# Optimization experiments

Measured on AMD Instinct MI355X. Metric: run time of the kernel, lower is better.

## Reference

```python
import jax, jax.numpy as jnp
import numpy as np

N = 8192       # num_nodes
E = 262144     # num_edges (avg degree 32)
D_IN = 256
D_H = 256
D_OUT = 256
BN_EPS = 1e-5


def _linear_params(key, din, dout):
    # torch nn.Linear default init: U(-1/sqrt(din), 1/sqrt(din))
    s = 1.0 / np.sqrt(din)
    kw, kb = jax.random.split(key)
    W = jax.random.uniform(kw, (dout, din), jnp.float32, -s, s)
    b = jax.random.uniform(kb, (dout,), jnp.float32, -s, s)
    return W, b


def setup_inputs() -> dict:
    key = jax.random.key(0)
    ks = jax.random.split(key, 6)
    x = jax.random.normal(ks[0], (N, D_IN), jnp.float32)
    edge_index = jax.random.randint(ks[1], (2, E), 0, N, dtype=jnp.int64)
    W1, b1 = _linear_params(ks[2], D_IN, D_H)
    W2, b2 = _linear_params(ks[3], D_H, D_H)
    W3, b3 = _linear_params(ks[4], D_H, D_OUT)
    return {
        "x": x, "edge_index": edge_index,
        "W1": W1, "b1": b1, "W2": W2, "b2": b2, "W3": W3, "b3": b3,
        "g1": jnp.ones((D_H,), jnp.float32), "be1": jnp.zeros((D_H,), jnp.float32),
        "g2": jnp.ones((D_H,), jnp.float32), "be2": jnp.zeros((D_H,), jnp.float32),
        "g3": jnp.ones((D_OUT,), jnp.float32), "be3": jnp.zeros((D_OUT,), jnp.float32),
    }


def _build_norm(edge_index):
    # add self loops, scatter 1.0 into dense NxN adjacency (duplicates collapse via set)
    loop = jnp.arange(N, dtype=edge_index.dtype)
    rows = jnp.concatenate([edge_index[0], loop])
    cols = jnp.concatenate([edge_index[1], loop])
    adj = jnp.zeros((N, N), jnp.float32).at[rows, cols].set(1.0)
    deg = adj.sum(axis=1)
    dinv = jnp.where(deg > 0, deg ** -0.5, 0.0)  # inf -> 0 as in original
    return dinv[:, None] * adj * dinv[None, :]


def _gcn(x, norm, W, b):
    # linear then symmetric-normalized aggregation
    return norm @ (x @ W.T + b)


def _bn(x, g, b):
    # BatchNorm1d with batch statistics (biased var), eps=1e-5
    mu = x.mean(axis=0)
    var = x.var(axis=0)
    return (x - mu) * jax.lax.rsqrt(var + BN_EPS) * g + b


def reference(x, edge_index, W1, b1, W2, b2, W3, b3, g1, be1, g2, be2, g3, be3):
    norm = _build_norm(edge_index)
    h = jax.nn.relu(_bn(_gcn(x, norm, W1, b1), g1, be1))
    h = jax.nn.relu(_bn(_gcn(h, norm, W2, b2), g2, be2))
    h = _bn(_gcn(h, norm, W3, b3), g3, be3)
    return h
```

## Files before the change

### kernel.cpp

```cpp
#include <hip/hip_runtime.h>

#define N_NODES 8192
#define N_EDGES 262144
#define D 256
#define ADJ_WORDS 256
#define MAX_DEG 128
#define AGG_BLOCKS 2048
#define RED_BLOCKS 128

typedef __attribute__((ext_vector_type(8))) short bf16x8;
typedef __attribute__((ext_vector_type(4))) float f32x4;

__device__ __forceinline__ short f2bf(float f) {
    unsigned u = __builtin_bit_cast(unsigned, f);
    u += 0x7fffu + ((u >> 16) & 1);
    return (short)(u >> 16);
}
__device__ __forceinline__ float bf2f(unsigned short u) {
    return __builtin_bit_cast(float, ((unsigned)u) << 16);
}

__global__ void build_adj(const int* __restrict__ ei, unsigned* __restrict__ adj,
                          int* __restrict__ deg) {
    int i = blockIdx.x * blockDim.x + threadIdx.x;
    int r, c;
    if (i < N_EDGES) {
        r = ei[i];
        c = ei[N_EDGES + i];
    } else if (i < N_EDGES + N_NODES) {
        r = i - N_EDGES;
        c = r;
    } else {
        return;
    }
    unsigned bit = 1u << (c & 31);
    unsigned old = atomicOr(&adj[r * ADJ_WORDS + (c >> 5)], bit);
    if (!(old & bit)) atomicAdd(&deg[r], 1);
}

__global__ __launch_bounds__(256) void build_nbrs(const unsigned* __restrict__ adj,
                                                  const int* __restrict__ deg,
                                                  int* __restrict__ nbr_idx,
                                                  float* __restrict__ nbr_w,
                                                  const float* __restrict__ W1,
                                                  const float* __restrict__ W2,
                                                  const float* __restrict__ W3,
                                                  unsigned short* __restrict__ Wb1,
                                                  unsigned short* __restrict__ Wb2,
                                                  unsigned short* __restrict__ Wb3) {
    if (blockIdx.x >= N_NODES) {
        int i = (blockIdx.x - N_NODES) * 256 + threadIdx.x;
        int which = i >> 16, j = i & 65535;
        const float* src = which == 0 ? W1 : which == 1 ? W2 : W3;
        unsigned short* dst = which == 0 ? Wb1 : which == 1 ? Wb2 : Wb3;
        dst[j] = (unsigned short)f2bf(src[j]);
        return;
    }
    const int r = blockIdx.x;
    const int t = threadIdx.x;
    const int lane = t & 63, wave = t >> 6;
    unsigned m = adj[r * ADJ_WORDS + t];
    int cnt = __popc(m);
    int x = cnt;
    #pragma unroll
    for (int off = 1; off < 64; off <<= 1) {
        int v = __shfl_up(x, off, 64);
        if (lane >= off) x += v;
    }
    __shared__ int wtot[4];
    if (lane == 63) wtot[wave] = x;
    __syncthreads();
    int woff = 0;
    #pragma unroll
    for (int w = 0; w < 4; w++) woff += (w < wave) ? wtot[w] : 0;
    int base = woff + x - cnt;
    const float dr = rsqrtf((float)deg[r]);
    int* oi = nbr_idx + (size_t)r * MAX_DEG;
    float* ow = nbr_w + (size_t)r * MAX_DEG;
    while (m) {
        int b = __ffs(m) - 1;
        m &= m - 1;
        int c = (t << 5) + b;
        if (base < MAX_DEG) {
            oi[base] = c;
            ow[base] = dr * rsqrtf((float)deg[c]);
        }
        base++;
    }
}

template <bool APPLY, bool RELU>
__global__ __launch_bounds__(256) void gemm_mfma(const float* __restrict__ Xsrc,
                                                 const float* __restrict__ psum2,
                                                 const float* __restrict__ psq2,
                                                 const float* __restrict__ g,
                                                 const float* __restrict__ be,
                                                 const unsigned short* __restrict__ Wb,
                                                 const float* __restrict__ bias,
                                                 unsigned short* __restrict__ Hb) {
    __shared__ float ssc[256], ssh[256];
    const int tid = threadIdx.x;
    if (APPLY) {
        float s = 0.f, q = 0.f;
        #pragma unroll 8
        for (int i = 0; i < RED_BLOCKS; i++) {
            s += psum2[i * 256 + tid];
            q += psq2[i * 256 + tid];
        }
        float mu = s * (1.0f / N_NODES);
        float var = q * (1.0f / N_NODES) - mu * mu;
        float rstd = rsqrtf(var + 1e-5f);
        float sc = g[tid] * rstd;
        ssc[tid] = sc;
        ssh[tid] = be[tid] - mu * sc;
        __syncthreads();
    }

    const int bn = blockIdx.x * 64;
    const int bm = blockIdx.y * 128;
    const int wave = tid >> 6, lane = tid & 63;
    const int l16 = lane & 15, q = lane >> 4;
    const int mrow0 = bm + wave * 32;

    f32x4 acc[2][4];
    #pragma unroll
    for (int i = 0; i < 2; i++)
        #pragma unroll
        for (int j = 0; j < 4; j++) acc[i][j] = (f32x4){0.f, 0.f, 0.f, 0.f};

    for (int k0 = 0; k0 < D; k0 += 32) {
        const int kq = k0 + q * 8;
        bf16x8 xb[2];
        float4 sc0, sc1, sh0, sh1;
        if (APPLY) {
            sc0 = *(const float4*)(ssc + kq);
            sc1 = *(const float4*)(ssc + kq + 4);
            sh0 = *(const float4*)(ssh + kq);
            sh1 = *(const float4*)(ssh + kq + 4);
        }
        #pragma unroll
        for (int mf = 0; mf < 2; mf++) {
            const float* xr = Xsrc + (size_t)(mrow0 + mf * 16 + l16) * D + kq;
            float4 a = *(const float4*)xr;
            float4 b = *(const float4*)(xr + 4);
            float v[8] = {a.x, a.y, a.z, a.w, b.x, b.y, b.z, b.w};
            if (APPLY) {
                float sc[8] = {sc0.x, sc0.y, sc0.z, sc0.w, sc1.x, sc1.y, sc1.z, sc1.w};
                float sh[8] = {sh0.x, sh0.y, sh0.z, sh0.w, sh1.x, sh1.y, sh1.z, sh1.w};
                #pragma unroll
                for (int j = 0; j < 8; j++) {
                    v[j] = fmaf(v[j], sc[j], sh[j]);
                    if (RELU) v[j] = fmaxf(v[j], 0.0f);
                }
            }
            #pragma unroll
            for (int j = 0; j < 8; j++) xb[mf][j] = f2bf(v[j]);
        }
        #pragma unroll
        for (int nf = 0; nf < 4; nf++) {
            bf16x8 wa = *(const bf16x8*)(Wb + (size_t)(bn + nf * 16 + l16) * D + kq);
            #pragma unroll
            for (int mf = 0; mf < 2; mf++)
                acc[mf][nf] = __builtin_amdgcn_mfma_f32_16x16x32_bf16(wa, xb[mf], acc[mf][nf], 0, 0, 0);
        }
    }

    #pragma unroll
    for (int mf = 0; mf < 2; mf++) {
        const int m = mrow0 + mf * 16 + l16;
        #pragma unroll
        for (int nf = 0; nf < 4; nf++) {
            const int nb = bn + nf * 16 + q * 4;
            float4 b4 = *(const float4*)(bias + nb);
            short4 o;
            o.x = f2bf(acc[mf][nf][0] + b4.x);
            o.y = f2bf(acc[mf][nf][1] + b4.y);
            o.z = f2bf(acc[mf][nf][2] + b4.z);
            o.w = f2bf(acc[mf][nf][3] + b4.w);
            *(short4*)(Hb + (size_t)m * D + nb) = o;
        }
    }
}

__global__ __launch_bounds__(256) void aggregate_bf16(const int* __restrict__ nbr_idx,
                                                      const float* __restrict__ nbr_w,
                                                      const int* __restrict__ deg,
                                                      const unsigned short* __restrict__ Hb,
                                                      float* __restrict__ G,
                                                      float* __restrict__ psum,
                                                      float* __restrict__ psumsq) {
    const int wave = threadIdx.x >> 6;
    const int lane = threadIdx.x & 63;
    const int ch = lane * 4;
    const int r = blockIdx.x * 4 + wave;

    int dg = deg[r]; if (dg > MAX_DEG) dg = MAX_DEG;
    const int* idx = nbr_idx + (size_t)r * MAX_DEG;
    const float* wt = nbr_w + (size_t)r * MAX_DEG;
    float4 A = make_float4(0.f, 0.f, 0.f, 0.f);
    int j = 0;
    for (; j + 8 <= dg; j += 8) {
        int4 c0 = *(const int4*)(idx + j);
        int4 c1 = *(const int4*)(idx + j + 4);
        float4 w0 = *(const float4*)(wt + j);
        float4 w1 = *(const float4*)(wt + j + 4);
        ushort4 u0 = *(const ushort4*)(Hb + (size_t)c0.x * D + ch);
        ushort4 u1 = *(const ushort4*)(Hb + (size_t)c0.y * D + ch);
        ushort4 u2 = *(const ushort4*)(Hb + (size_t)c0.z * D + ch);
        ushort4 u3 = *(const ushort4*)(Hb + (size_t)c0.w * D + ch);
        ushort4 u4 = *(const ushort4*)(Hb + (size_t)c1.x * D + ch);
        ushort4 u5 = *(const ushort4*)(Hb + (size_t)c1.y * D + ch);
        ushort4 u6 = *(const ushort4*)(Hb + (size_t)c1.z * D + ch);
        ushort4 u7 = *(const ushort4*)(Hb + (size_t)c1.w * D + ch);
        A.x = fmaf(w0.x, bf2f(u0.x), A.x); A.y = fmaf(w0.x, bf2f(u0.y), A.y);
        A.z = fmaf(w0.x, bf2f(u0.z), A.z); A.w = fmaf(w0.x, bf2f(u0.w), A.w);
        A.x = fmaf(w0.y, bf2f(u1.x), A.x); A.y = fmaf(w0.y, bf2f(u1.y), A.y);
        A.z = fmaf(w0.y, bf2f(u1.z), A.z); A.w = fmaf(w0.y, bf2f(u1.w), A.w);
        A.x = fmaf(w0.z, bf2f(u2.x), A.x); A.y = fmaf(w0.z, bf2f(u2.y), A.y);
        A.z = fmaf(w0.z, bf2f(u2.z), A.z); A.w = fmaf(w0.z, bf2f(u2.w), A.w);
        A.x = fmaf(w0.w, bf2f(u3.x), A.x); A.y = fmaf(w0.w, bf2f(u3.y), A.y);
        A.z = fmaf(w0.w, bf2f(u3.z), A.z); A.w = fmaf(w0.w, bf2f(u3.w), A.w);
        A.x = fmaf(w1.x, bf2f(u4.x), A.x); A.y = fmaf(w1.x, bf2f(u4.y), A.y);
        A.z = fmaf(w1.x, bf2f(u4.z), A.z); A.w = fmaf(w1.x, bf2f(u4.w), A.w);
        A.x = fmaf(w1.y, bf2f(u5.x), A.x); A.y = fmaf(w1.y, bf2f(u5.y), A.y);
        A.z = fmaf(w1.y, bf2f(u5.z), A.z); A.w = fmaf(w1.y, bf2f(u5.w), A.w);
        A.x = fmaf(w1.z, bf2f(u6.x), A.x); A.y = fmaf(w1.z, bf2f(u6.y), A.y);
        A.z = fmaf(w1.z, bf2f(u6.z), A.z); A.w = fmaf(w1.z, bf2f(u6.w), A.w);
        A.x = fmaf(w1.w, bf2f(u7.x), A.x); A.y = fmaf(w1.w, bf2f(u7.y), A.y);
        A.z = fmaf(w1.w, bf2f(u7.z), A.z); A.w = fmaf(w1.w, bf2f(u7.w), A.w);
    }
    for (; j + 4 <= dg; j += 4) {
        int4 c0 = *(const int4*)(idx + j);
        float4 w0 = *(const float4*)(wt + j);
        ushort4 u0 = *(const ushort4*)(Hb + (size_t)c0.x * D + ch);
        ushort4 u1 = *(const ushort4*)(Hb + (size_t)c0.y * D + ch);
        ushort4 u2 = *(const ushort4*)(Hb + (size_t)c0.z * D + ch);
        ushort4 u3 = *(const ushort4*)(Hb + (size_t)c0.w * D + ch);
        A.x = fmaf(w0.x, bf2f(u0.x), A.x); A.y = fmaf(w0.x, bf2f(u0.y), A.y);
        A.z = fmaf(w0.x, bf2f(u0.z), A.z); A.w = fmaf(w0.x, bf2f(u0.w), A.w);
        A.x = fmaf(w0.y, bf2f(u1.x), A.x); A.y = fmaf(w0.y, bf2f(u1.y), A.y);
        A.z = fmaf(w0.y, bf2f(u1.z), A.z); A.w = fmaf(w0.y, bf2f(u1.w), A.w);
        A.x = fmaf(w0.z, bf2f(u2.x), A.x); A.y = fmaf(w0.z, bf2f(u2.y), A.y);
        A.z = fmaf(w0.z, bf2f(u2.z), A.z); A.w = fmaf(w0.z, bf2f(u2.w), A.w);
        A.x = fmaf(w0.w, bf2f(u3.x), A.x); A.y = fmaf(w0.w, bf2f(u3.y), A.y);
        A.z = fmaf(w0.w, bf2f(u3.z), A.z); A.w = fmaf(w0.w, bf2f(u3.w), A.w);
    }
    for (; j < dg; j++) {
        int c = idx[j];
        float w = wt[j];
        ushort4 u = *(const ushort4*)(Hb + (size_t)c * D + ch);
        A.x = fmaf(w, bf2f(u.x), A.x); A.y = fmaf(w, bf2f(u.y), A.y);
        A.z = fmaf(w, bf2f(u.z), A.z); A.w = fmaf(w, bf2f(u.w), A.w);
    }
    *(float4*)(G + (size_t)r * D + ch) = A;

    __shared__ float ls[4][256], lss[4][256];
    ls[wave][ch] = A.x; ls[wave][ch + 1] = A.y; ls[wave][ch + 2] = A.z; ls[wave][ch + 3] = A.w;
    lss[wave][ch] = A.x * A.x; lss[wave][ch + 1] = A.y * A.y;
    lss[wave][ch + 2] = A.z * A.z; lss[wave][ch + 3] = A.w * A.w;
    __syncthreads();
    const int t = threadIdx.x;
    psum[blockIdx.x * 256 + t] = ls[0][t] + ls[1][t] + ls[2][t] + ls[3][t];
    psumsq[blockIdx.x * 256 + t] = lss[0][t] + lss[1][t] + lss[2][t] + lss[3][t];
}

__global__ __launch_bounds__(256) void reduce_partials(const float* __restrict__ psum,
                                                       const float* __restrict__ psumsq,
                                                       float* __restrict__ psum2,
                                                       float* __restrict__ psumsq2) {
    const int b = blockIdx.x;
    const int t = threadIdx.x;
    const int rows = AGG_BLOCKS / RED_BLOCKS;
    float s = 0.0f, q = 0.0f;
    #pragma unroll
    for (int i = 0; i < rows; i++) {
        s += psum[(size_t)(b * rows + i) * 256 + t];
        q += psumsq[(size_t)(b * rows + i) * 256 + t];
    }
    psum2[b * 256 + t] = s;
    psumsq2[b * 256 + t] = q;
}

__global__ __launch_bounds__(256) void bn_apply_out(const float* __restrict__ G,
                                                    const float* __restrict__ psum2,
                                                    const float* __restrict__ psq2,
                                                    const float* __restrict__ g,
                                                    const float* __restrict__ be,
                                                    float* __restrict__ Out) {
    __shared__ float ssc[256], ssh[256];
    const int tid = threadIdx.x;
    {
        float s = 0.f, q = 0.f;
        #pragma unroll 8
        for (int i = 0; i < RED_BLOCKS; i++) {
            s += psum2[i * 256 + tid];
            q += psq2[i * 256 + tid];
        }
        float mu = s * (1.0f / N_NODES);
        float var = q * (1.0f / N_NODES) - mu * mu;
        float rstd = rsqrtf(var + 1e-5f);
        float sc = g[tid] * rstd;
        ssc[tid] = sc;
        ssh[tid] = be[tid] - mu * sc;
        __syncthreads();
    }
    const int rows_per_block = 64;
    const int r0 = blockIdx.x * rows_per_block;
    const int ch = (tid & 63) * 4;
    const int rsub = tid >> 6;
    float4 sc = *(const float4*)(ssc + ch);
    float4 sh = *(const float4*)(ssh + ch);
    for (int rr = rsub; rr < rows_per_block; rr += 4) {
        const size_t off = (size_t)(r0 + rr) * D + ch;
        float4 v = *(const float4*)(G + off);
        v.x = fmaf(v.x, sc.x, sh.x);
        v.y = fmaf(v.y, sc.y, sh.y);
        v.z = fmaf(v.z, sc.z, sh.z);
        v.w = fmaf(v.w, sc.w, sh.w);
        *(float4*)(Out + off) = v;
    }
}

extern "C" void kernel_launch(void* const* d_in, const int* in_sizes, int n_in,
                              void* d_out, int out_size, void* d_ws, size_t ws_size,
                              hipStream_t stream) {
    const float* x  = (const float*)d_in[0];
    const int*   ei = (const int*)d_in[1];
    const float* W1 = (const float*)d_in[2];
    const float* b1 = (const float*)d_in[3];
    const float* W2 = (const float*)d_in[4];
    const float* b2 = (const float*)d_in[5];
    const float* W3 = (const float*)d_in[6];
    const float* b3 = (const float*)d_in[7];
    const float* g1 = (const float*)d_in[8];
    const float* be1 = (const float*)d_in[9];
    const float* g2 = (const float*)d_in[10];
    const float* be2 = (const float*)d_in[11];
    const float* g3 = (const float*)d_in[12];
    const float* be3 = (const float*)d_in[13];

    char* ws = (char*)d_ws;
    unsigned*       adj  = (unsigned*)ws;
    unsigned short* Hb   = (unsigned short*)ws;
    int*            deg  = (int*)(ws + (8 << 20));
    float*          psum2= (float*)(ws + (8 << 20) + (64 << 10));
    float*          psq2 = (float*)(ws + (8 << 20) + (192 << 10));
    unsigned short* Wb1  = (unsigned short*)(ws + (8 << 20) + (320 << 10));
    unsigned short* Wb2  = (unsigned short*)(ws + (8 << 20) + (448 << 10));
    unsigned short* Wb3  = (unsigned short*)(ws + (8 << 20) + (576 << 10));
    float*          psum = (float*)(ws + (9 << 20));
    float*          psq  = (float*)(ws + (11 << 20));
    int*            nbr_idx = (int*)  (ws + (13 << 20));
    float*          nbr_w   = (float*)(ws + (17 << 20));
    float*          G       = (float*)(ws + (21 << 20));

    hipMemsetAsync(ws, 0, (8 << 20) + (32 << 10), stream);

    build_adj<<<(N_EDGES + N_NODES + 255) / 256, 256, 0, stream>>>(ei, adj, deg);
    build_nbrs<<<N_NODES + 768, 256, 0, stream>>>(adj, deg, nbr_idx, nbr_w,
                                                  W1, W2, W3, Wb1, Wb2, Wb3);

    dim3 ggrid(D / 64, N_NODES / 128);

    gemm_mfma<false, false><<<ggrid, 256, 0, stream>>>(x, nullptr, nullptr, nullptr, nullptr,
                                                       Wb1, b1, Hb);
    aggregate_bf16<<<AGG_BLOCKS, 256, 0, stream>>>(nbr_idx, nbr_w, deg, Hb, G, psum, psq);
    reduce_partials<<<RED_BLOCKS, 256, 0, stream>>>(psum, psq, psum2, psq2);

    gemm_mfma<true, true><<<ggrid, 256, 0, stream>>>(G, psum2, psq2, g1, be1, Wb2, b2, Hb);
    aggregate_bf16<<<AGG_BLOCKS, 256, 0, stream>>>(nbr_idx, nbr_w, deg, Hb, G, psum, psq);
    reduce_partials<<<RED_BLOCKS, 256, 0, stream>>>(psum, psq, psum2, psq2);

    gemm_mfma<true, true><<<ggrid, 256, 0, stream>>>(G, psum2, psq2, g2, be2, Wb3, b3, Hb);
    aggregate_bf16<<<AGG_BLOCKS, 256, 0, stream>>>(nbr_idx, nbr_w, deg, Hb, G, psum, psq);
    reduce_partials<<<RED_BLOCKS, 256, 0, stream>>>(psum, psq, psum2, psq2);

    bn_apply_out<<<N_NODES / 64, 256, 0, stream>>>(G, psum2, psq2, g3, be3, (float*)d_out);
}
```

Baseline: 237.1 us.

## Fuse launches: merge weight cast into adj build, gemm1 with nbr list, atomic BN partials

The bf16 weight conversion moves into build_adj and the first GEMM shares one launch with the neighbor-list build, since the two are independent. The three reduce_partials kernels are removed: each aggregate block atomically adds its column sums into one of 16 zeroed partial rows, and the consumers then sum only 16 rows. Hb gets its own workspace region because it no longer aliases adj. This cuts kernel launches and global partial traffic at the cost of atomic contention and a larger memset.

```diff
diff --git a/kernel.cpp b/kernel.cpp
--- a/kernel.cpp
+++ b/kernel.cpp
@@ -6,7 +6,7 @@
 #define ADJ_WORDS 256
 #define MAX_DEG 128
 #define AGG_BLOCKS 2048
-#define RED_BLOCKS 128
+#define NPART 16
 
 typedef __attribute__((ext_vector_type(8))) short bf16x8;
 typedef __attribute__((ext_vector_type(4))) float f32x4;
@@ -20,43 +20,41 @@
     return __builtin_bit_cast(float, ((unsigned)u) << 16);
 }
 
-__global__ void build_adj(const int* __restrict__ ei, unsigned* __restrict__ adj,
-                          int* __restrict__ deg) {
-    int i = blockIdx.x * blockDim.x + threadIdx.x;
+__global__ __launch_bounds__(256) void build_adj(const int* __restrict__ ei,
+                                                 unsigned* __restrict__ adj,
+                                                 int* __restrict__ deg,
+                                                 const float* __restrict__ W1,
+                                                 const float* __restrict__ W2,
+                                                 const float* __restrict__ W3,
+                                                 unsigned short* __restrict__ Wb1,
+                                                 unsigned short* __restrict__ Wb2,
+                                                 unsigned short* __restrict__ Wb3) {
+    int i = blockIdx.x * 256 + threadIdx.x;
+    if (i >= N_EDGES + N_NODES) {
+        int j = i - (N_EDGES + N_NODES);
+        int which = j >> 16, k = j & 65535;
+        const float* src = which == 0 ? W1 : which == 1 ? W2 : W3;
+        unsigned short* dst = which == 0 ? Wb1 : which == 1 ? Wb2 : Wb3;
+        dst[k] = (unsigned short)f2bf(src[k]);
+        return;
+    }
     int r, c;
     if (i < N_EDGES) {
         r = ei[i];
         c = ei[N_EDGES + i];
-    } else if (i < N_EDGES + N_NODES) {
+    } else {
         r = i - N_EDGES;
         c = r;
-    } else {
-        return;
     }
     unsigned bit = 1u << (c & 31);
     unsigned old = atomicOr(&adj[r * ADJ_WORDS + (c >> 5)], bit);
     if (!(old & bit)) atomicAdd(&deg[r], 1);
 }
 
-__global__ __launch_bounds__(256) void build_nbrs(const unsigned* __restrict__ adj,
-                                                  const int* __restrict__ deg,
-                                                  int* __restrict__ nbr_idx,
-                                                  float* __restrict__ nbr_w,
-                                                  const float* __restrict__ W1,
-                                                  const float* __restrict__ W2,
-                                                  const float* __restrict__ W3,
-                                                  unsigned short* __restrict__ Wb1,
-                                                  unsigned short* __restrict__ Wb2,
-                                                  unsigned short* __restrict__ Wb3) {
-    if (blockIdx.x >= N_NODES) {
-        int i = (blockIdx.x - N_NODES) * 256 + threadIdx.x;
-        int which = i >> 16, j = i & 65535;
-        const float* src = which == 0 ? W1 : which == 1 ? W2 : W3;
-        unsigned short* dst = which == 0 ? Wb1 : which == 1 ? Wb2 : Wb3;
-        dst[j] = (unsigned short)f2bf(src[j]);
-        return;
-    }
-    const int r = blockIdx.x;
+__device__ __forceinline__ void nbrs_body(const unsigned* __restrict__ adj,
+                                          const int* __restrict__ deg,
+                                          int* __restrict__ nbr_idx,
+                                          float* __restrict__ nbr_w, int r) {
     const int t = threadIdx.x;
     const int lane = t & 63, wave = t >> 6;
     unsigned m = adj[r * ADJ_WORDS + t];
@@ -90,22 +88,23 @@
 }
 
 template <bool APPLY, bool RELU>
-__global__ __launch_bounds__(256) void gemm_mfma(const float* __restrict__ Xsrc,
-                                                 const float* __restrict__ psum2,
-                                                 const float* __restrict__ psq2,
-                                                 const float* __restrict__ g,
-                                                 const float* __restrict__ be,
-                                                 const unsigned short* __restrict__ Wb,
-                                                 const float* __restrict__ bias,
-                                                 unsigned short* __restrict__ Hb) {
+__device__ __forceinline__ void gemm_body(const float* __restrict__ Xsrc,
+                                          const float* __restrict__ psA,
+                                          const float* __restrict__ psQ,
+                                          const float* __restrict__ g,
+                                          const float* __restrict__ be,
+                                          const unsigned short* __restrict__ Wb,
+                                          const float* __restrict__ bias,
+                                          unsigned short* __restrict__ Hb,
+                                          int bn, int bm) {
     __shared__ float ssc[256], ssh[256];
     const int tid = threadIdx.x;
     if (APPLY) {
         float s = 0.f, q = 0.f;
-        #pragma unroll 8
-        for (int i = 0; i < RED_BLOCKS; i++) {
-            s += psum2[i * 256 + tid];
-            q += psq2[i * 256 + tid];
+        #pragma unroll
+        for (int i = 0; i < NPART; i++) {
+            s += psA[i * 256 + tid];
+            q += psQ[i * 256 + tid];
         }
         float mu = s * (1.0f / N_NODES);
         float var = q * (1.0f / N_NODES) - mu * mu;
@@ -116,8 +115,6 @@
         __syncthreads();
     }
 
-    const int bn = blockIdx.x * 64;
-    const int bm = blockIdx.y * 128;
     const int wave = tid >> 6, lane = tid & 63;
     const int l16 = lane & 15, q = lane >> 4;
     const int mrow0 = bm + wave * 32;
@@ -182,13 +179,42 @@
     }
 }
 
+__global__ __launch_bounds__(256) void gemm1_and_nbrs(const float* __restrict__ x,
+                                                      const unsigned short* __restrict__ Wb1,
+                                                      const float* __restrict__ b1,
+                                                      unsigned short* __restrict__ Hb,
+                                                      const unsigned* __restrict__ adj,
+                                                      const int* __restrict__ deg,
+                                                      int* __restrict__ nbr_idx,
+                                                      float* __restrict__ nbr_w) {
+    const int bg = blockIdx.x;
+    if (bg < 256) {
+        gemm_body<false, false>(x, nullptr, nullptr, nullptr, nullptr, Wb1, b1, Hb,
+                                (bg & 3) * 64, (bg >> 2) * 128);
+    } else {
+        nbrs_body(adj, deg, nbr_idx, nbr_w, bg - 256);
+    }
+}
+
+__global__ __launch_bounds__(256) void gemm_mfma_bn(const float* __restrict__ Xsrc,
+                                                    const float* __restrict__ psA,
+                                                    const float* __restrict__ psQ,
+                                                    const float* __restrict__ g,
+                                                    const float* __restrict__ be,
+                                                    const unsigned short* __restrict__ Wb,
+                                                    const float* __restrict__ bias,
+                                                    unsigned short* __restrict__ Hb) {
+    gemm_body<true, true>(Xsrc, psA, psQ, g, be, Wb, bias, Hb,
+                          blockIdx.x * 64, blockIdx.y * 128);
+}
+
 __global__ __launch_bounds__(256) void aggregate_bf16(const int* __restrict__ nbr_idx,
                                                       const float* __restrict__ nbr_w,
                                                       const int* __restrict__ deg,
                                                       const unsigned short* __restrict__ Hb,
                                                       float* __restrict__ G,
-                                                      float* __restrict__ psum,
-                                                      float* __restrict__ psumsq) {
+                                                      float* __restrict__ psA,
+                                                      float* __restrict__ psQ) {
     const int wave = threadIdx.x >> 6;
     const int lane = threadIdx.x & 63;
     const int ch = lane * 4;
@@ -260,30 +286,14 @@
     lss[wave][ch + 2] = A.z * A.z; lss[wave][ch + 3] = A.w * A.w;
     __syncthreads();
     const int t = threadIdx.x;
-    psum[blockIdx.x * 256 + t] = ls[0][t] + ls[1][t] + ls[2][t] + ls[3][t];
-    psumsq[blockIdx.x * 256 + t] = lss[0][t] + lss[1][t] + lss[2][t] + lss[3][t];
-}
-
-__global__ __launch_bounds__(256) void reduce_partials(const float* __restrict__ psum,
-                                                       const float* __restrict__ psumsq,
-                                                       float* __restrict__ psum2,
-                                                       float* __restrict__ psumsq2) {
-    const int b = blockIdx.x;
-    const int t = threadIdx.x;
-    const int rows = AGG_BLOCKS / RED_BLOCKS;
-    float s = 0.0f, q = 0.0f;
-    #pragma unroll
-    for (int i = 0; i < rows; i++) {
-        s += psum[(size_t)(b * rows + i) * 256 + t];
-        q += psumsq[(size_t)(b * rows + i) * 256 + t];
-    }
-    psum2[b * 256 + t] = s;
-    psumsq2[b * 256 + t] = q;
+    const int prow = (blockIdx.x & (NPART - 1)) * 256;
+    atomicAdd(&psA[prow + t], ls[0][t] + ls[1][t] + ls[2][t] + ls[3][t]);
+    atomicAdd(&psQ[prow + t], lss[0][t] + lss[1][t] + lss[2][t] + lss[3][t]);
 }
 
 __global__ __launch_bounds__(256) void bn_apply_out(const float* __restrict__ G,
-                                                    const float* __restrict__ psum2,
-                                                    const float* __restrict__ psq2,
+                                                    const float* __restrict__ psA,
+                                                    const float* __restrict__ psQ,
                                                     const float* __restrict__ g,
                                                     const float* __restrict__ be,
                                                     float* __restrict__ Out) {
@@ -291,10 +301,10 @@
     const int tid = threadIdx.x;
     {
         float s = 0.f, q = 0.f;
-        #pragma unroll 8
-        for (int i = 0; i < RED_BLOCKS; i++) {
-            s += psum2[i * 256 + tid];
-            q += psq2[i * 256 + tid];
+        #pragma unroll
+        for (int i = 0; i < NPART; i++) {
+            s += psA[i * 256 + tid];
+            q += psQ[i * 256 + tid];
         }
         float mu = s * (1.0f / N_NODES);
         float var = q * (1.0f / N_NODES) - mu * mu;
@@ -341,39 +351,35 @@
 
     char* ws = (char*)d_ws;
     unsigned*       adj  = (unsigned*)ws;
-    unsigned short* Hb   = (unsigned short*)ws;
     int*            deg  = (int*)(ws + (8 << 20));
-    float*          psum2= (float*)(ws + (8 << 20) + (64 << 10));
-    float*          psq2 = (float*)(ws + (8 << 20) + (192 << 10));
-    unsigned short* Wb1  = (unsigned short*)(ws + (8 << 20) + (320 << 10));
-    unsigned short* Wb2  = (unsigned short*)(ws + (8 << 20) + (448 << 10));
-    unsigned short* Wb3  = (unsigned short*)(ws + (8 << 20) + (576 << 10));
-    float*          psum = (float*)(ws + (9 << 20));
-    float*          psq  = (float*)(ws + (11 << 20));
-    int*            nbr_idx = (int*)  (ws + (13 << 20));
-    float*          nbr_w   = (float*)(ws + (17 << 20));
-    float*          G       = (float*)(ws + (21 << 20));
-
-    hipMemsetAsync(ws, 0, (8 << 20) + (32 << 10), stream);
-
-    build_adj<<<(N_EDGES + N_NODES + 255) / 256, 256, 0, stream>>>(ei, adj, deg);
-    build_nbrs<<<N_NODES + 768, 256, 0, stream>>>(adj, deg, nbr_idx, nbr_w,
-                                                  W1, W2, W3, Wb1, Wb2, Wb3);
+    float*          psA0 = (float*)(ws + (8 << 20) + (32 << 10));
+    float*          psQ0 = psA0 + NPART * 256;
+    float*          psA1 = psQ0 + NPART * 256;
+    float*          psQ1 = psA1 + NPART * 256;
+    float*          psA2 = psQ1 + NPART * 256;
+    float*          psQ2 = psA2 + NPART * 256;
+    unsigned short* Wb1  = (unsigned short*)(ws + (8 << 20) + (128 << 10));
+    unsigned short* Wb2  = (unsigned short*)(ws + (8 << 20) + (256 << 10));
+    unsigned short* Wb3  = (unsigned short*)(ws + (8 << 20) + (384 << 10));
+    int*            nbr_idx = (int*)  (ws + (9 << 20));
+    float*          nbr_w   = (float*)(ws + (13 << 20));
+    float*          G       = (float*)(ws + (17 << 20));
+    unsigned short* Hb      = (unsigned short*)(ws + (25 << 20));
+
+    hipMemsetAsync(ws, 0, (8 << 20) + (128 << 10), stream);
+
+    build_adj<<<1824, 256, 0, stream>>>(ei, adj, deg, W1, W2, W3, Wb1, Wb2, Wb3);
+
+    gemm1_and_nbrs<<<256 + N_NODES, 256, 0, stream>>>(x, Wb1, b1, Hb, adj, deg, nbr_idx, nbr_w);
+    aggregate_bf16<<<AGG_BLOCKS, 256, 0, stream>>>(nbr_idx, nbr_w, deg, Hb, G, psA0, psQ0);
 
     dim3 ggrid(D / 64, N_NODES / 128);
 
-    gemm_mfma<false, false><<<ggrid, 256, 0, stream>>>(x, nullptr, nullptr, nullptr, nullptr,
-                                                       Wb1, b1, Hb);
-    aggregate_bf16<<<AGG_BLOCKS, 256, 0, stream>>>(nbr_idx, nbr_w, deg, Hb, G, psum, psq);
-    reduce_partials<<<RED_BLOCKS, 256, 0, stream>>>(psum, psq, psum2, psq2);
-
-    gemm_mfma<true, true><<<ggrid, 256, 0, stream>>>(G, psum2, psq2, g1, be1, Wb2, b2, Hb);
-    aggregate_bf16<<<AGG_BLOCKS, 256, 0, stream>>>(nbr_idx, nbr_w, deg, Hb, G, psum, psq);
-    reduce_partials<<<RED_BLOCKS, 256, 0, stream>>>(psum, psq, psum2, psq2);
-
-    gemm_mfma<true, true><<<ggrid, 256, 0, stream>>>(G, psum2, psq2, g2, be2, Wb3, b3, Hb);
-    aggregate_bf16<<<AGG_BLOCKS, 256, 0, stream>>>(nbr_idx, nbr_w, deg, Hb, G, psum, psq);
-    reduce_partials<<<RED_BLOCKS, 256, 0, stream>>>(psum, psq, psum2, psq2);
-
-    bn_apply_out<<<N_NODES / 64, 256, 0, stream>>>(G, psum2, psq2, g3, be3, (float*)d_out);
-}
+    gemm_mfma_bn<<<ggrid, 256, 0, stream>>>(G, psA0, psQ0, g1, be1, Wb2, b2, Hb);
+    aggregate_bf16<<<AGG_BLOCKS, 256, 0, stream>>>(nbr_idx, nbr_w, deg, Hb, G, psA1, psQ1);
+
+    gemm_mfma_bn<<<ggrid, 256, 0, stream>>>(G, psA1, psQ1, g2, be2, Wb3, b3, Hb);
+    aggregate_bf16<<<AGG_BLOCKS, 256, 0, stream>>>(nbr_idx, nbr_w, deg, Hb, G, psA2, psQ2);
+
+    bn_apply_out<<<N_NODES / 64, 256, 0, stream>>>(G, psA2, psQ2, g3, be3, (float*)d_out);
+}
```

After: 226.9 us. 4.3% less time.
